# Optimization experiments

Hardware: AMD Instinct MI355X
Metric: run time of the kernel (lower is better)

Reference implementation:

```python
import jax, jax.numpy as jnp
import numpy as np

N_TOKEN = 267735
CUTOFFS = [20000, 40000, 200000, 267735]
ENDS = [0] + CUTOFFS
CLUSTER_DIMS = [1024, 256, 64, 16]   # d_embed // div_val**i
CLUSTER_SIZES = [20000, 20000, 160000, 67735]
D_PROJ = 1024
T, B = 256, 4
N_CLUSTERS = 3


def setup_inputs() -> dict:
    key = jax.random.key(0)
    ks = jax.random.split(key, 16)
    inp = {}
    inp["hidden"] = jax.random.normal(ks[0], (T, B, D_PROJ), jnp.float32)
    inp["target"] = jax.random.randint(ks[1], (T, B), 0, N_TOKEN)
    for i in range(4):
        inp[f"W{i}"] = jax.random.normal(ks[2 + 3 * i], (CLUSTER_SIZES[i], CLUSTER_DIMS[i]), jnp.float32) * 0.02
        inp[f"b{i}"] = jnp.zeros((CLUSTER_SIZES[i],), jnp.float32)
        inp[f"P{i}"] = jax.random.normal(ks[3 + 3 * i], (CLUSTER_DIMS[i], D_PROJ), jnp.float32) * 0.02
    inp["cluster_weight"] = jax.random.normal(ks[14], (N_CLUSTERS, 1024), jnp.float32) * 0.02
    inp["cluster_bias"] = jnp.zeros((N_CLUSTERS,), jnp.float32)
    return inp


def _logit(x, W, b, P):
    # x: [T,B,d_proj], P: [e,d_proj], W: [n,e] -> [T,B,n]
    y = jnp.einsum('ibd,ed->ibe', x, P)
    return jnp.einsum('ibe,ne->ibn', y, W) + b


def _gather(logprob, tgt):
    # pick logprob[t, b, tgt[t,b]]
    return jnp.take_along_axis(logprob, tgt[..., None], axis=-1)[..., 0]


def reference(hidden, target, W0, b0, P0, W1, b1, P1, W2, b2, P2, W3, b3, P3,
              cluster_weight, cluster_bias):
    Ws = [W0, W1, W2, W3]
    bs = [b0, b1, b2, b3]
    Ps = [P0, P1, P2, P3]
    loss = jnp.zeros(target.shape, jnp.float32)
    head_logprob = None
    for i in range(4):
        l_idx, r_idx = ENDS[i], ENDS[i + 1]
        mask = (target >= l_idx) & (target < r_idx)
        cur_t = jnp.maximum(jnp.minimum(target, r_idx - 1) - l_idx, 0)
        if i == 0:
            Wh = jnp.concatenate([W0, cluster_weight], axis=0)
            bh = jnp.concatenate([b0, cluster_bias], axis=0)
            head_logprob = jax.nn.log_softmax(_logit(hidden, Wh, bh, P0), axis=-1)
            cur_loss = _gather(head_logprob, cur_t)
        else:
            tail_logprob = jax.nn.log_softmax(_logit(hidden, Ws[i], bs[i], Ps[i]), axis=-1)
            logprob_i = head_logprob[..., CUTOFFS[0] + i - 1, None] + tail_logprob
            cur_loss = _gather(logprob_i, cur_t)
        loss = jnp.where(mask, cur_loss, loss)
    return jnp.mean(-loss)
```

## Files before the change

### kernel.cpp

```cpp
#include <hip/hip_runtime.h>
#include <math.h>

typedef short short8 __attribute__((ext_vector_type(8)));
typedef float f32x4 __attribute__((ext_vector_type(4)));
typedef unsigned long long u64;

#define LOG2E 1.4426950408889634f

__device__ __forceinline__ unsigned short f2bf_rne(float f) {
    unsigned u = __float_as_uint(f);
    unsigned r = (u + 0x7fff + ((u >> 16) & 1)) >> 16;
    return (unsigned short)r;
}
__device__ __forceinline__ float bf2f(unsigned short h) {
    return __uint_as_float(((unsigned)h) << 16);
}
__device__ __forceinline__ void load_lds16(const void* g, void* l) {
    __builtin_amdgcn_global_load_lds((const __attribute__((address_space(1))) void*)g,
                                     (__attribute__((address_space(3))) void*)l,
                                     16, 0, 0);
}
template<int N>
__device__ __forceinline__ void waitvm() {
    asm volatile("s_waitcnt vmcnt(%0)" :: "n"(N) : "memory");
}
__device__ __forceinline__ u64 pack8_fp8(const float* v, float s) {
    int lo = 0, hi = 0;
    lo = __builtin_amdgcn_cvt_pk_fp8_f32(v[0] * s, v[1] * s, lo, false);
    lo = __builtin_amdgcn_cvt_pk_fp8_f32(v[2] * s, v[3] * s, lo, true);
    hi = __builtin_amdgcn_cvt_pk_fp8_f32(v[4] * s, v[5] * s, hi, false);
    hi = __builtin_amdgcn_cvt_pk_fp8_f32(v[6] * s, v[7] * s, hi, true);
    return (u64)(unsigned)lo | ((u64)(unsigned)hi << 32);
}

__global__ void cvt_h(const float* __restrict__ in, unsigned short* __restrict__ out)
{
    const int i = blockIdx.x * 256 + threadIdx.x;
    const float4 v = *(const float4*)(in + (size_t)i * 4);
    ushort4 h;
    h.x = f2bf_rne(v.x); h.y = f2bf_rne(v.y);
    h.z = f2bf_rne(v.z); h.w = f2bf_rne(v.w);
    *(ushort4*)(out + (size_t)i * 4) = h;
}

struct ProjDesc {
    const float* B;
    unsigned short* Cbf;
    unsigned char* Cf8;
    int ldc; int nreal; int N; int Kpad; int gy_begin;
};

__global__ __launch_bounds__(256) void prepproj(
    const unsigned short* __restrict__ A,
    ProjDesc p0, ProjDesc p1, ProjDesc p2, ProjDesc p3,
    const float* __restrict__ W0, const float* __restrict__ cw,
    const float* __restrict__ W1, const float* __restrict__ W2,
    const float* __restrict__ W3,
    const float* __restrict__ b0, const float* __restrict__ cb,
    const float* __restrict__ b1, const float* __restrict__ b2,
    const float* __restrict__ b3,
    unsigned char* __restrict__ Wb0, unsigned char* __restrict__ Wb1,
    unsigned char* __restrict__ Wb2, unsigned char* __restrict__ Wb3,
    float* __restrict__ bp)
{
    __shared__ char smem[34816];

    const int tid = threadIdx.x;
    const int bx = blockIdx.x;

    if (bx >= 96) {
        const unsigned E0 = 1286144u;
        const unsigned E1 = 1613824u;
        const unsigned E2 = 2260992u;
        const unsigned E3 = 2539520u;
        const unsigned E4 = 2607520u;
        const unsigned stride = (gridDim.x - 96) * 256u;
        for (unsigned u = (bx - 96) * 256u + tid; u < E4; u += stride) {
            if (u < E3) {
                const float* src = nullptr;
                unsigned char* dstm; unsigned tile, kg2, r, tstride;
                if (u < E0) {
                    tile = u >> 13; const unsigned rem = u & 8191u;
                    kg2 = rem >> 7; r = rem & 127u;
                    const unsigned row = tile * 128u + r;
                    if (row < 20000u)      src = W0 + (size_t)row * 1024 + kg2 * 16;
                    else if (row < 20003u) src = cw + (size_t)(row - 20000u) * 1024 + kg2 * 16;
                    dstm = Wb0; tstride = 131072u;
                } else if (u < E1) {
                    const unsigned j = u - E0;
                    tile = j >> 11; const unsigned rem = j & 2047u;
                    kg2 = rem >> 7; r = rem & 127u;
                    const unsigned row = tile * 128u + r;
                    if (row < 20000u) src = W1 + (size_t)row * 256 + kg2 * 16;
                    dstm = Wb1; tstride = 32768u;
                } else if (u < E2) {
                    const unsigned j = u - E1;
                    tile = j >> 9; kg2 = (j >> 7) & 3u; r = j & 127u;
                    const unsigned row = tile * 128u + r;
                    if (row < 160000u) src = W2 + (size_t)row * 64 + kg2 * 16;
                    dstm = Wb2; tstride = 8192u;
                } else {
                    const unsigned j = u - E2;
                    tile = j >> 9; kg2 = (j >> 7) & 3u; r = j & 127u;
                    const unsigned row = tile * 128u + r;
                    if (kg2 == 0 && row < 67735u) src = W3 + (size_t)row * 16;
                    dstm = Wb3; tstride = 8192u;
                }
                float f[16];
                if (src) {
#pragma unroll
                    for (int q = 0; q < 4; ++q) {
                        const float4 v = *(const float4*)(src + q * 4);
                        f[q * 4 + 0] = v.x; f[q * 4 + 1] = v.y;
                        f[q * 4 + 2] = v.z; f[q * 4 + 3] = v.w;
                    }
                } else {
#pragma unroll
                    for (int q = 0; q < 16; ++q) f[q] = 0.f;
                }
                u64* dst = (u64*)(dstm + (size_t)tile * tstride);
                dst[(2 * kg2) * 128 + r]     = pack8_fp8(f,     16.0f);
                dst[(2 * kg2 + 1) * 128 + r] = pack8_fp8(f + 8, 16.0f);
            } else {
                const unsigned idx0 = (u - E3) * 4u;
                float e[4];
#pragma unroll
                for (int j = 0; j < 4; ++j) {
                    const unsigned idx = idx0 + j;
                    float v;
                    if (idx < 20096u) {
                        v = (idx < 20000u) ? b0[idx] * LOG2E
                          : (idx < 20003u) ? cb[idx - 20000u] * LOG2E : -1e30f;
                    } else if (idx < 40576u) {
                        const unsigned i1 = idx - 20096u;
                        v = (i1 < 20000u) ? b1[i1] * LOG2E : -1e30f;
                    } else if (idx < 202368u) {
                        const unsigned i2 = idx - 40576u;
                        v = (i2 < 160000u) ? b2[i2] * LOG2E : -1e30f;
                    } else {
                        const unsigned i3 = idx - 202368u;
                        v = (i3 < 67735u) ? b3[i3] * LOG2E : -1e30f;
                    }
                    e[j] = v;
                }
                *(float4*)(bp + idx0) = make_float4(e[0], e[1], e[2], e[3]);
            }
        }
        return;
    }

    unsigned short* As = (unsigned short*)smem;
    unsigned short* Bs = (unsigned short*)(smem + 16384);

    const int mt = bx & 7;
    const int py = bx >> 3;
    ProjDesc p = (py >= p3.gy_begin) ? p3 : (py >= p2.gy_begin) ? p2
               : (py >= p1.gy_begin) ? p1 : p0;

    const int w = tid >> 6;
    const int l = tid & 63;
    const int m0 = mt * 128;
    const int n0 = (py - p.gy_begin) * 128;
    const int wm = (w >> 1) * 64;
    const int wn = (w & 1) * 64;
    const int lane16 = l & 15;
    const int quad = l >> 4;

    const unsigned short* aptr[4];
    int ag_base[4];
#pragma unroll
    for (int i = 0; i < 4; ++i) {
        const int g = w * 256 + i * 64 + l;
        aptr[i] = A + (size_t)(m0 + (g & 127)) * 1024 + (g >> 7) * 8;
        ag_base[i] = (w * 256 + i * 64) * 8;
    }

    const int bn = tid >> 1;
    const int bhalf = tid & 1;
    int brow = n0 + bn;
    if (brow > p.N - 1) brow = p.N - 1;
    const float* brow_ptr = p.B + (size_t)brow * 1024;

    f32x4 acc[4][4] = {};

    for (int k0 = 0; k0 < 1024; k0 += 64) {
        __syncthreads();
#pragma unroll
        for (int i = 0; i < 4; ++i)
            load_lds16(aptr[i] + k0, (void*)&As[ag_base[i]]);
#pragma unroll
        for (int j = 0; j < 8; ++j) {
            const int kq = bhalf * 8 + j;
            const float4 v = *(const float4*)(brow_ptr + k0 + kq * 4);
            const unsigned px = __builtin_amdgcn_perm(__float_as_uint(v.y), __float_as_uint(v.x), 0x07060302);
            const unsigned pyv = __builtin_amdgcn_perm(__float_as_uint(v.w), __float_as_uint(v.z), 0x07060302);
            const int gran = (kq >> 1) * 128 + bn;
            *(uint2*)&Bs[gran * 8 + (kq & 1) * 4] = make_uint2(px, pyv);
        }
        __syncthreads();

#pragma unroll
        for (int kk = 0; kk < 2; ++kk) {
            const int kgb = kk * 4 + quad;
            short8 af[4], bfr[4];
#pragma unroll
            for (int mi = 0; mi < 4; ++mi)
                af[mi] = *(const short8*)&As[(kgb * 128 + wm + mi * 16 + lane16) * 8];
#pragma unroll
            for (int ni = 0; ni < 4; ++ni)
                bfr[ni] = *(const short8*)&Bs[(kgb * 128 + wn + ni * 16 + lane16) * 8];
#pragma unroll
            for (int mi = 0; mi < 4; ++mi)
#pragma unroll
                for (int ni = 0; ni < 4; ++ni)
                    acc[mi][ni] = __builtin_amdgcn_mfma_f32_16x16x32_bf16(
                        af[mi], bfr[ni], acc[mi][ni], 0, 0, 0);
        }
    }

#pragma unroll
    for (int mi = 0; mi < 4; ++mi)
#pragma unroll
        for (int ni = 0; ni < 4; ++ni) {
            const int n = n0 + wn + ni * 16 + lane16;
            if (n < p.ldc) {
#pragma unroll
                for (int r = 0; r < 4; ++r) {
                    const int m = m0 + wm + mi * 16 + quad * 4 + r;
                    const float v = (n < p.nreal) ? acc[mi][ni][r] : 0.f;
                    p.Cbf[(size_t)m * p.ldc + n] = f2bf_rne(v);
                }
            }
        }

    float* bounce = (float*)smem;
    u64* Yout = (u64*)p.Cf8 + (size_t)mt * 16 * p.Kpad;
    for (int c = 0; c < 2; ++c) {
        const int colbase = n0 + c * 64;
        if (colbase >= p.Kpad) break;
        __syncthreads();
        if ((w & 1) == c) {
#pragma unroll
            for (int mi = 0; mi < 4; ++mi)
#pragma unroll
                for (int ni = 0; ni < 4; ++ni) {
                    const int ncol = ni * 16 + lane16;
                    const bool real = (colbase + ncol) < p.nreal;
#pragma unroll
                    for (int r = 0; r < 4; ++r) {
                        const int m = wm + mi * 16 + quad * 4 + r;
                        bounce[m * 66 + ncol] = real ? acc[mi][ni][r] : 0.f;
                    }
                }
        }
        __syncthreads();
#pragma unroll
        for (int i = 0; i < 4; ++i) {
            const int g = i * 256 + tid;
            const int kgl = g >> 7;
            const int m = g & 127;
            float v[8];
#pragma unroll
            for (int j = 0; j < 8; ++j) v[j] = bounce[m * 66 + kgl * 8 + j];
            Yout[((colbase >> 3) + kgl) * 128 + m] = pack8_fp8(v, 4.0f);
        }
    }
}

struct ExpDesc {
    const unsigned char* A;
    const unsigned char* W;
    const float* bias;
    float* part;
    int Kpad; int ksl; int kmask; int gy_begin; int slab;
};

__global__ __launch_bounds__(256) void exp_gemm(ExpDesc d0, ExpDesc d1, ExpDesc d2, ExpDesc d3)
{
    __shared__ u64 As[2][1024];
    __shared__ u64 Bs[2][1024];
    __shared__ float biasLds[2048];

    const int mt = blockIdx.x;
    const int gy = blockIdx.y;

    ExpDesc d = (gy >= d3.gy_begin) ? d3 : (gy >= d2.gy_begin) ? d2
              : (gy >= d1.gy_begin) ? d1 : d0;

    const int tid = threadIdx.x;
    const int w = tid >> 6;
    const int l = tid & 63;
    const int wm = (w >> 1) * 64;
    const int wn = (w & 1) * 64;
    const int lane16 = l & 15;
    const int quad = l >> 4;

    const int tiles_begin = (gy - d.gy_begin) * d.slab;
    const int T = d.slab << d.ksl;
    const int kmask = d.kmask;
    const int ksl = d.ksl;
    const bool haveA = (kmask != 0);

    const size_t tstride = (size_t)128 * d.Kpad;
    const unsigned char* Abase = d.A + (size_t)mt * tstride;
    const unsigned char* Bbase = d.W + (size_t)tiles_begin * tstride;

    const int so0 = tid * 16;
    const int so1 = 4096 + tid * 16;

    {
        const float* bsrc = d.bias + (size_t)tiles_begin * 128;
        const int nb = d.slab * 32;
        for (int u = tid; u < nb; u += 256)
            load_lds16(bsrc + u * 4, (char*)biasLds + u * 16);
    }
    load_lds16(Abase + so0, (char*)As[0] + so0);
    load_lds16(Abase + so1, (char*)As[0] + so1);
    load_lds16(Bbase + so0, (char*)Bs[0] + so0);
    load_lds16(Bbase + so1, (char*)Bs[0] + so1);
    {
        const int kc = 1 & kmask;
        if (haveA) {
            const unsigned char* ac = Abase + kc * 8192;
            load_lds16(ac + so0, (char*)As[1] + so0);
            load_lds16(ac + so1, (char*)As[1] + so1);
        }
        const unsigned char* bc = Bbase + (size_t)(1 >> ksl) * tstride + kc * 8192;
        load_lds16(bc + so0, (char*)Bs[1] + so0);
        load_lds16(bc + so1, (char*)Bs[1] + so1);
    }

    f32x4 acc[4][4] = {};
    float rowsum[4][4] = {};
    const float c1 = LOG2E / 64.0f;

    for (int it = 0; it < T; ++it) {
        const int slot = it & 1;
        if (it + 1 < T) { if (haveA) waitvm<4>(); else waitvm<2>(); }
        else            { waitvm<0>(); }
        __builtin_amdgcn_s_barrier();
        __builtin_amdgcn_sched_barrier(0);

        const u64* Ar = haveA ? As[slot] : As[0];
        const u64* Br = Bs[slot];
#pragma unroll
        for (int ks = 0; ks < 2; ++ks) {
            u64 af[4], bfr[4];
#pragma unroll
            for (int mi = 0; mi < 4; ++mi)
                af[mi] = Ar[(ks * 4 + quad) * 128 + wm + mi * 16 + lane16];
#pragma unroll
            for (int ni = 0; ni < 4; ++ni)
                bfr[ni] = Br[(ks * 4 + quad) * 128 + wn + ni * 16 + lane16];
#pragma unroll
            for (int mi = 0; mi < 4; ++mi)
#pragma unroll
                for (int ni = 0; ni < 4; ++ni)
                    acc[mi][ni] = __builtin_amdgcn_mfma_f32_16x16x32_fp8_fp8(
                        (long)af[mi], (long)bfr[ni], acc[mi][ni], 0, 0, 0);
        }

        if ((it & kmask) == kmask) {
            const int tile = it >> ksl;
            float biasc[4];
#pragma unroll
            for (int ni = 0; ni < 4; ++ni)
                biasc[ni] = biasLds[tile * 128 + wn + ni * 16 + lane16];
#pragma unroll
            for (int mi = 0; mi < 4; ++mi)
#pragma unroll
                for (int r = 0; r < 4; ++r) {
                    float s = exp2f(fmaf(acc[mi][0][r], c1, biasc[0]))
                            + exp2f(fmaf(acc[mi][1][r], c1, biasc[1]))
                            + exp2f(fmaf(acc[mi][2][r], c1, biasc[2]))
                            + exp2f(fmaf(acc[mi][3][r], c1, biasc[3]));
                    rowsum[mi][r] += s;
                }
#pragma unroll
            for (int mi = 0; mi < 4; ++mi)
#pragma unroll
                for (int ni = 0; ni < 4; ++ni)
                    acc[mi][ni] = (f32x4){0.f, 0.f, 0.f, 0.f};
        }

        __builtin_amdgcn_sched_barrier(0);
        __builtin_amdgcn_s_barrier();

        if (it + 2 < T) {
            const int nit = it + 2;
            const int kc = nit & kmask;
            if (haveA) {
                const unsigned char* ac = Abase + kc * 8192;
                load_lds16(ac + so0, (char*)As[slot] + so0);
                load_lds16(ac + so1, (char*)As[slot] + so1);
            }
            const unsigned char* bc = Bbase + (size_t)(nit >> ksl) * tstride + kc * 8192;
            load_lds16(bc + so0, (char*)Bs[slot] + so0);
            load_lds16(bc + so1, (char*)Bs[slot] + so1);
        }
    }

#pragma unroll
    for (int off = 1; off < 16; off <<= 1)
#pragma unroll
        for (int mi = 0; mi < 4; ++mi)
#pragma unroll
            for (int r = 0; r < 4; ++r)
                rowsum[mi][r] += __shfl_xor(rowsum[mi][r], off, 64);

    __syncthreads();
    float* buf = (float*)As;
    if (lane16 == 0) {
#pragma unroll
        for (int mi = 0; mi < 4; ++mi)
#pragma unroll
            for (int r = 0; r < 4; ++r)
                buf[(wm + mi * 16 + quad * 4 + r) * 2 + (wn >> 6)] = rowsum[mi][r];
    }
    __syncthreads();
    if (tid < 128)
        d.part[(size_t)(gy - d.gy_begin) * 1024 + mt * 128 + tid] = buf[tid * 2 + 0] + buf[tid * 2 + 1];
}

__global__ void redext(const float* __restrict__ p0, const float* __restrict__ p1,
                       const float* __restrict__ p2, const float* __restrict__ p3,
                       float* __restrict__ S,
                       const unsigned short* __restrict__ Y0, const unsigned short* __restrict__ Y1,
                       const unsigned short* __restrict__ Y2, const unsigned short* __restrict__ Y3,
                       const int* __restrict__ target,
                       const float* __restrict__ W0, const float* __restrict__ b0,
                       const float* __restrict__ W1, const float* __restrict__ b1,
                       const float* __restrict__ W2, const float* __restrict__ b2,
                       const float* __restrict__ W3, const float* __restrict__ b3,
                       const float* __restrict__ cw, const float* __restrict__ cb,
                       float* __restrict__ headlogit, float* __restrict__ taillogit)
{
    if (blockIdx.x < 16) {
        const int idx = blockIdx.x * 256 + threadIdx.x;
        const int c = idx >> 10, m = idx & 1023;
        const float* p = (c == 0) ? p0 : (c == 1) ? p1 : (c == 2) ? p2 : p3;
        const int G = (c == 0) ? 157 : (c == 1) ? 40 : (c == 2) ? 79 : 34;
        float s = 0.f;
        for (int y = 0; y < G; ++y) s += p[(size_t)y * 1024 + m];
        S[idx] = s;
        return;
    }
    const int token = (blockIdx.x - 16) * 4 + (threadIdx.x >> 6);
    const int lane = threadIdx.x & 63;
    const int tgt = target[token];
    const int ci = (tgt < 20000) ? 0 : (tgt < 40000) ? 1 : (tgt < 200000) ? 2 : 3;

    {
        const int h = (ci == 0) ? tgt : (20000 + ci - 1);
        const float* row;
        float bb;
        if (h < 20000) { row = W0 + (size_t)h * 1024; bb = b0[h]; }
        else           { row = cw + (size_t)(h - 20000) * 1024; bb = cb[h - 20000]; }
        const unsigned short* y = Y0 + (size_t)token * 1024;
        float s = 0.f;
        for (int k = lane; k < 1024; k += 64) s += bf2f(y[k]) * row[k];
#pragma unroll
        for (int off = 1; off < 64; off <<= 1) s += __shfl_xor(s, off, 64);
        if (lane == 0) headlogit[token] = s + bb;
    }

    float tl = 0.f;
    if (ci > 0) {
        const unsigned short* Y; const float* W; const float* b; int K, ldy, lidx;
        if (ci == 1)      { Y = Y1; W = W1; b = b1; K = 256; ldy = 256; lidx = 20000; }
        else if (ci == 2) { Y = Y2; W = W2; b = b2; K = 64;  ldy = 64;  lidx = 40000; }
        else              { Y = Y3; W = W3; b = b3; K = 16;  ldy = 64;  lidx = 200000; }
        const int r = tgt - lidx;
        const unsigned short* y = Y + (size_t)token * ldy;
        const float* row = W + (size_t)r * K;
        float s = 0.f;
        for (int k = lane; k < K; k += 64) s += bf2f(y[k]) * row[k];
#pragma unroll
        for (int off = 1; off < 64; off <<= 1) s += __shfl_xor(s, off, 64);
        tl = s + b[r];
    }
    if (lane == 0) taillogit[token] = tl;
}

__global__ void finalize_kernel(const float* __restrict__ S,
                                const int* __restrict__ target,
                                const float* __restrict__ headlogit,
                                const float* __restrict__ taillogit,
                                float* __restrict__ out)
{
    __shared__ float red[256];
    const int tid = threadIdx.x;
    float acc = 0.f;
    for (int token = tid; token < 1024; token += 256) {
        const int tgt = target[token];
        const int ci = (tgt < 20000) ? 0 : (tgt < 40000) ? 1 : (tgt < 200000) ? 2 : 3;
        float lp = headlogit[token] - logf(S[token]);
        if (ci > 0)
            lp += taillogit[token] - logf(S[ci * 1024 + token]);
        acc -= lp;
    }
    red[tid] = acc;
    __syncthreads();
    for (int s = 128; s > 0; s >>= 1) {
        if (tid < s) red[tid] += red[tid + s];
        __syncthreads();
    }
    if (tid == 0) out[0] = red[0] * (1.0f / 1024.0f);
}

extern "C" void kernel_launch(void* const* d_in, const int* in_sizes, int n_in,
                              void* d_out, int out_size, void* d_ws, size_t ws_size,
                              hipStream_t stream)
{
    const float* hidden = (const float*)d_in[0];
    const int*   target = (const int*)d_in[1];
    const float* W0 = (const float*)d_in[2];  const float* b0 = (const float*)d_in[3];  const float* P0 = (const float*)d_in[4];
    const float* W1 = (const float*)d_in[5];  const float* b1 = (const float*)d_in[6];  const float* P1 = (const float*)d_in[7];
    const float* W2 = (const float*)d_in[8];  const float* b2 = (const float*)d_in[9];  const float* P2 = (const float*)d_in[10];
    const float* W3 = (const float*)d_in[11]; const float* b3 = (const float*)d_in[12]; const float* P3 = (const float*)d_in[13];
    const float* cw = (const float*)d_in[14]; const float* cb = (const float*)d_in[15];
    float* out = (float*)d_out;

    unsigned char* ws = (unsigned char*)d_ws;
    unsigned short* h_bf = (unsigned short*)ws;
    unsigned short* Y0bf = (unsigned short*)(ws + 2097152);
    unsigned short* Y1bf = (unsigned short*)(ws + 4194304);
    unsigned short* Y2bf = (unsigned short*)(ws + 4718592);
    unsigned short* Y3bf = (unsigned short*)(ws + 4849664);
    unsigned char* Y0f8 = ws + 4980736;
    unsigned char* Y1f8 = ws + 6029312;
    unsigned char* Y2f8 = ws + 6291456;
    unsigned char* Y3f8 = ws + 6356992;
    unsigned char* Wb0 = ws + 6422528;
    unsigned char* Wb1 = ws + 27000832;
    unsigned char* Wb2 = ws + 32243712;
    unsigned char* Wb3 = ws + 42598400;
    float* bp = (float*)(ws + 47054848);

    float* part0 = (float*)ws;
    float* part1 = part0 + (size_t)157 * 1024;
    float* part2 = part1 + (size_t)40 * 1024;
    float* part3 = part2 + (size_t)79 * 1024;
    float* S = part3 + (size_t)34 * 1024;
    float* headlogit = S + 4096;
    float* taillogit = headlogit + 1024;

    cvt_h<<<1024, 256, 0, stream>>>(hidden, h_bf);

    ProjDesc pr0 = { P0, Y0bf, Y0f8, 1024, 1024, 1024, 1024, 0 };
    ProjDesc pr1 = { P1, Y1bf, Y1f8, 256,  256,  256,  256,  8 };
    ProjDesc pr2 = { P2, Y2bf, Y2f8, 64,   64,   64,   64,   10 };
    ProjDesc pr3 = { P3, Y3bf, Y3f8, 64,   16,   16,   64,   11 };
    prepproj<<<2048, 256, 0, stream>>>(h_bf, pr0, pr1, pr2, pr3,
                                       W0, cw, W1, W2, W3,
                                       b0, cb, b1, b2, b3,
                                       Wb0, Wb1, Wb2, Wb3, bp);

    ExpDesc d0 = { Y0f8, Wb0, bp,          part0, 1024, 4, 15, 0,   1 };
    ExpDesc d1 = { Y1f8, Wb1, bp + 20096,  part1, 256,  2, 3,  157, 4 };
    ExpDesc d2 = { Y2f8, Wb2, bp + 40576,  part2, 64,   0, 0,  197, 16 };
    ExpDesc d3 = { Y3f8, Wb3, bp + 202368, part3, 64,   0, 0,  276, 16 };
    exp_gemm<<<dim3(8, 310), 256, 0, stream>>>(d0, d1, d2, d3);

    redext<<<272, 256, 0, stream>>>(part0, part1, part2, part3, S,
                                    Y0bf, Y1bf, Y2bf, Y3bf, target,
                                    W0, b0, W1, b1, W2, b2, W3, b3,
                                    cw, cb, headlogit, taillogit);

    finalize_kernel<<<1, 256, 0, stream>>>(S, target, headlogit, taillogit, out);
}
```

Measured before the change: 426.6 us.

## Double M tile per block in exp_gemm to share W tiles across two row groups

Each exp_gemm block now has 512 threads (8 waves) and covers two 128-row M tiles (p and p+4), so every W tile loaded into LDS is reused by both halves. The grid shrinks from 8 to 4 blocks in x, which halves the global/L2 traffic for the large weight matrices that dominate this GEMM. The cost is a larger LDS footprint and higher register pressure per block, fewer blocks in total, and modified vmcnt waits that must match the new load counts.

```diff
diff --git a/kernel.cpp b/kernel.cpp
--- a/kernel.cpp
+++ b/kernel.cpp
@@ -275,13 +275,13 @@
     int Kpad; int ksl; int kmask; int gy_begin; int slab;
 };
 
-__global__ __launch_bounds__(256) void exp_gemm(ExpDesc d0, ExpDesc d1, ExpDesc d2, ExpDesc d3)
+__global__ __launch_bounds__(512) void exp_gemm(ExpDesc d0, ExpDesc d1, ExpDesc d2, ExpDesc d3)
 {
-    __shared__ u64 As[2][1024];
+    __shared__ u64 As[2][2048];
     __shared__ u64 Bs[2][1024];
     __shared__ float biasLds[2048];
 
-    const int mt = blockIdx.x;
+    const int p = blockIdx.x;
     const int gy = blockIdx.y;
 
     ExpDesc d = (gy >= d3.gy_begin) ? d3 : (gy >= d2.gy_begin) ? d2
@@ -290,8 +290,10 @@
     const int tid = threadIdx.x;
     const int w = tid >> 6;
     const int l = tid & 63;
-    const int wm = (w >> 1) * 64;
-    const int wn = (w & 1) * 64;
+    const int wmt = w >> 2;
+    const int wq = w & 3;
+    const int wm = (wq >> 1) * 64;
+    const int wn = (wq & 1) * 64;
     const int lane16 = l & 15;
     const int quad = l >> 4;
 
@@ -302,32 +304,30 @@
     const bool haveA = (kmask != 0);
 
     const size_t tstride = (size_t)128 * d.Kpad;
-    const unsigned char* Abase = d.A + (size_t)mt * tstride;
+    const unsigned char* Abase0 = d.A + (size_t)p * tstride;
+    const unsigned char* Abase1 = d.A + (size_t)(p + 4) * tstride;
     const unsigned char* Bbase = d.W + (size_t)tiles_begin * tstride;
 
-    const int so0 = tid * 16;
-    const int so1 = 4096 + tid * 16;
+    const int so = tid * 16;
 
     {
         const float* bsrc = d.bias + (size_t)tiles_begin * 128;
         const int nb = d.slab * 32;
-        for (int u = tid; u < nb; u += 256)
+        for (int u = tid; u < nb; u += 512)
             load_lds16(bsrc + u * 4, (char*)biasLds + u * 16);
     }
-    load_lds16(Abase + so0, (char*)As[0] + so0);
-    load_lds16(Abase + so1, (char*)As[0] + so1);
-    load_lds16(Bbase + so0, (char*)Bs[0] + so0);
-    load_lds16(Bbase + so1, (char*)Bs[0] + so1);
-    {
-        const int kc = 1 & kmask;
-        if (haveA) {
-            const unsigned char* ac = Abase + kc * 8192;
-            load_lds16(ac + so0, (char*)As[1] + so0);
-            load_lds16(ac + so1, (char*)As[1] + so1);
-        }
-        const unsigned char* bc = Bbase + (size_t)(1 >> ksl) * tstride + kc * 8192;
-        load_lds16(bc + so0, (char*)Bs[1] + so0);
-        load_lds16(bc + so1, (char*)Bs[1] + so1);
+    if (haveA) {
+        load_lds16(Abase0 + so, (char*)As[0] + so);
+        load_lds16(Abase1 + so, (char*)As[0] + 8192 + so);
+        load_lds16(Bbase + so, (char*)Bs[0] + so);
+        load_lds16(Abase0 + 8192 + so, (char*)As[1] + so);
+        load_lds16(Abase1 + 8192 + so, (char*)As[1] + 8192 + so);
+        load_lds16(Bbase + (size_t)(1 >> ksl) * tstride + 8192 + so, (char*)Bs[1] + so);
+    } else {
+        load_lds16(Abase0 + so, (char*)As[0] + so);
+        load_lds16(Abase1 + so, (char*)As[0] + 8192 + so);
+        load_lds16(Bbase + so, (char*)Bs[0] + so);
+        load_lds16(Bbase + tstride + so, (char*)Bs[1] + so);
     }
 
     f32x4 acc[4][4] = {};
@@ -336,12 +336,12 @@
 
     for (int it = 0; it < T; ++it) {
         const int slot = it & 1;
-        if (it + 1 < T) { if (haveA) waitvm<4>(); else waitvm<2>(); }
+        if (it + 1 < T) { if (haveA) waitvm<3>(); else waitvm<1>(); }
         else            { waitvm<0>(); }
         __builtin_amdgcn_s_barrier();
         __builtin_amdgcn_sched_barrier(0);
 
-        const u64* Ar = haveA ? As[slot] : As[0];
+        const u64* Ar = (haveA ? As[slot] : As[0]) + wmt * 1024;
         const u64* Br = Bs[slot];
 #pragma unroll
         for (int ks = 0; ks < 2; ++ks) {
@@ -390,13 +390,11 @@
             const int nit = it + 2;
             const int kc = nit & kmask;
             if (haveA) {
-                const unsigned char* ac = Abase + kc * 8192;
-                load_lds16(ac + so0, (char*)As[slot] + so0);
-                load_lds16(ac + so1, (char*)As[slot] + so1);
+                load_lds16(Abase0 + kc * 8192 + so, (char*)As[slot] + so);
+                load_lds16(Abase1 + kc * 8192 + so, (char*)As[slot] + 8192 + so);
             }
             const unsigned char* bc = Bbase + (size_t)(nit >> ksl) * tstride + kc * 8192;
-            load_lds16(bc + so0, (char*)Bs[slot] + so0);
-            load_lds16(bc + so1, (char*)Bs[slot] + so1);
+            load_lds16(bc + so, (char*)Bs[slot] + so);
         }
     }
 
@@ -415,11 +413,15 @@
         for (int mi = 0; mi < 4; ++mi)
 #pragma unroll
             for (int r = 0; r < 4; ++r)
-                buf[(wm + mi * 16 + quad * 4 + r) * 2 + (wn >> 6)] = rowsum[mi][r];
+                buf[(wmt * 128 + wm + mi * 16 + quad * 4 + r) * 2 + (wn >> 6)] = rowsum[mi][r];
     }
     __syncthreads();
-    if (tid < 128)
-        d.part[(size_t)(gy - d.gy_begin) * 1024 + mt * 128 + tid] = buf[tid * 2 + 0] + buf[tid * 2 + 1];
+    if (tid < 256) {
+        const int row = tid & 127;
+        const int mtreal = p + (tid >> 7) * 4;
+        d.part[(size_t)(gy - d.gy_begin) * 1024 + mtreal * 128 + row] =
+            buf[tid * 2 + 0] + buf[tid * 2 + 1];
+    }
 }
 
 __global__ void redext(const float* __restrict__ p0, const float* __restrict__ p1,
@@ -560,7 +562,7 @@
     ExpDesc d1 = { Y1f8, Wb1, bp + 20096,  part1, 256,  2, 3,  157, 4 };
     ExpDesc d2 = { Y2f8, Wb2, bp + 40576,  part2, 64,   0, 0,  197, 16 };
     ExpDesc d3 = { Y3f8, Wb3, bp + 202368, part3, 64,   0, 0,  276, 16 };
-    exp_gemm<<<dim3(8, 310), 256, 0, stream>>>(d0, d1, d2, d3);
+    exp_gemm<<<dim3(4, 310), 512, 0, stream>>>(d0, d1, d2, d3);
 
     redext<<<272, 256, 0, stream>>>(part0, part1, part2, part3, S,
                                     Y0bf, Y1bf, Y2bf, Y3bf, target,
```

New measurement: 395.0 us. 7.4% less time.
